# Kernel optimization log

Measured on AMD Instinct MI355X. Metric: run time of the kernel, lower is better.

The kernel has to match this reference:

```python
import jax, jax.numpy as jnp
import numpy as np

D_IN = 1024
D_OUT = 1024
NUM_HEADS = 16
HEAD_DIM = D_OUT // NUM_HEADS


def setup_inputs() -> dict:
    key = jax.random.key(0)
    ks = jax.random.split(key, 6)
    scale = 0.02
    x = jax.random.normal(ks[0], (2, 2048, D_IN), dtype=jnp.float32)
    Wq = jax.random.normal(ks[1], (D_IN, D_OUT), dtype=jnp.float32) * scale
    Wk = jax.random.normal(ks[2], (D_IN, D_OUT), dtype=jnp.float32) * scale
    Wv = jax.random.normal(ks[3], (D_IN, D_OUT), dtype=jnp.float32) * scale
    Wo = jax.random.normal(ks[4], (D_OUT, D_OUT), dtype=jnp.float32) * scale
    bo = jax.random.normal(ks[5], (D_OUT,), dtype=jnp.float32) * scale
    return {"x": x, "Wq": Wq, "Wk": Wk, "Wv": Wv, "Wo": Wo, "bo": bo}


def reference(x, Wq, Wk, Wv, Wo, bo):
    b, T, _ = x.shape
    h, dh = NUM_HEADS, HEAD_DIM
    # QKV projections (no bias), split heads: [b,T,d_out] -> [b,h,T,dh]
    q = (x @ Wq).reshape(b, T, h, dh).transpose(0, 2, 1, 3)
    k = (x @ Wk).reshape(b, T, h, dh).transpose(0, 2, 1, 3)
    v = (x @ Wv).reshape(b, T, h, dh).transpose(0, 2, 1, 3)
    # scaled dot-product scores with causal mask
    scores = jnp.einsum("bhqd,bhkd->bhqk", q, k) / jnp.sqrt(jnp.float32(dh))
    causal = jnp.tril(jnp.ones((T, T), dtype=bool))  # True = allowed
    scores = jnp.where(causal, scores, -jnp.inf)
    attn = jax.nn.softmax(scores, axis=-1)
    # dropout p=0.0 -> identity
    ctx = jnp.einsum("bhqk,bhkd->bhqd", attn, v)
    ctx = ctx.transpose(0, 2, 1, 3).reshape(b, T, h * dh)
    return ctx @ Wo + bo
```

## Files before the change

kernel.cpp:

```cpp
#include <hip/hip_runtime.h>

typedef __attribute__((ext_vector_type(8))) __bf16 bf16x8;
typedef __attribute__((ext_vector_type(4))) __bf16 bf16x4;
typedef __attribute__((ext_vector_type(4))) float  f32x4;

static constexpr int TSEQ    = 2048;
static constexpr int DMODEL  = 1024;
static constexpr int HD      = 64;
static constexpr int VSTRIDE = 2080;
static constexpr int LSTR    = 72;

__global__ __launch_bounds__(256) void k_convert_x(const float* __restrict__ x,
                                                   __bf16* __restrict__ xbf) {
  size_t i = ((size_t)blockIdx.x * 256 + threadIdx.x) * 4;
  float4 v = *(const float4*)(x + i);
  bf16x4 o = { (__bf16)v.x, (__bf16)v.y, (__bf16)v.z, (__bf16)v.w };
  *(bf16x4*)(xbf + i) = o;
}

__global__ __launch_bounds__(1024) void k_transpose_w(const float* __restrict__ w0,
    const float* __restrict__ w1, const float* __restrict__ w2,
    const float* __restrict__ w3, __bf16* __restrict__ wt_all) {
  __shared__ float tile[32][33];
  const float* w = blockIdx.z == 0 ? w0 : blockIdx.z == 1 ? w1 : blockIdx.z == 2 ? w2 : w3;
  __bf16* out = wt_all + (size_t)blockIdx.z * DMODEL * DMODEL;
  int n0 = blockIdx.x * 32, k0 = blockIdx.y * 32;
  int tx = threadIdx.x, ty = threadIdx.y;
  tile[ty][tx] = w[(size_t)(k0 + ty) * DMODEL + n0 + tx];
  __syncthreads();
  out[(size_t)(n0 + ty) * DMODEL + k0 + tx] = (__bf16)tile[tx][ty];
}

__device__ __forceinline__ void gemm_mainloop(const __bf16* __restrict__ A,
                                              const __bf16* __restrict__ Bt,
                                              int bm, int bn,
                                              __bf16* At, __bf16* Bl,
                                              f32x4 acc[4][4]) {
  const int tid  = threadIdx.x;
  const int lane = tid & 63;
  const int l15  = lane & 15, quad = lane >> 4;
  const int wv   = tid >> 6;
  const int wm   = (wv >> 1) * 64, wn = (wv & 1) * 64;
  const int s0   = wv * 2;
  const int srow = lane >> 2;
  const int scol = (lane & 3) << 3;
  for (int k0 = 0; k0 < 1024; k0 += 32) {
    __syncthreads();
#pragma unroll
    for (int ss = 0; ss < 2; ss++) {
      const int s   = s0 + ss;
      const int row = s * 16 + srow;
      const __bf16* ga = A  + (size_t)(bm + row) * 1024 + k0 + scol;
      const __bf16* gb = Bt + (size_t)(bn + row) * 1024 + k0 + scol;
      __builtin_amdgcn_global_load_lds(
          (const __attribute__((address_space(1))) void*)ga,
          (__attribute__((address_space(3))) void*)(At + s * 512), 16, 0, 0);
      __builtin_amdgcn_global_load_lds(
          (const __attribute__((address_space(1))) void*)gb,
          (__attribute__((address_space(3))) void*)(Bl + s * 512), 16, 0, 0);
    }
    __syncthreads();
    bf16x8 af[4], bfr[4];
#pragma unroll
    for (int mt = 0; mt < 4; mt++)
      af[mt] = *(const bf16x8*)(At + (wm + mt * 16 + l15) * 32 + quad * 8);
#pragma unroll
    for (int nt = 0; nt < 4; nt++)
      bfr[nt] = *(const bf16x8*)(Bl + (wn + nt * 16 + l15) * 32 + quad * 8);
#pragma unroll
    for (int mt = 0; mt < 4; mt++)
#pragma unroll
      for (int nt = 0; nt < 4; nt++)
        acc[mt][nt] = __builtin_amdgcn_mfma_f32_16x16x32_bf16(
            af[mt], bfr[nt], acc[mt][nt], 0, 0, 0);
  }
}

__global__ __launch_bounds__(256) void k_gemm_qkv(const __bf16* __restrict__ xbf,
    const __bf16* __restrict__ wt_all, __bf16* __restrict__ qws,
    __bf16* __restrict__ kws, __bf16* __restrict__ vtws) {
  __shared__ __bf16 At[128 * 32];
  __shared__ __bf16 Bl[128 * 32];
  const int which = blockIdx.z;
  const __bf16* wt = wt_all + (size_t)which * DMODEL * DMODEL;
  const int bm = blockIdx.y * 128, bn = blockIdx.x * 128;
  f32x4 acc[4][4];
  const f32x4 z = {0.f, 0.f, 0.f, 0.f};
#pragma unroll
  for (int mt = 0; mt < 4; mt++)
#pragma unroll
    for (int nt = 0; nt < 4; nt++) acc[mt][nt] = z;
  gemm_mainloop(xbf, wt, bm, bn, At, Bl, acc);
  const int lane = threadIdx.x & 63;
  const int l15 = lane & 15, quad = lane >> 4;
  const int wv = threadIdx.x >> 6;
  const int wm = (wv >> 1) * 64, wn = (wv & 1) * 64;
#pragma unroll
  for (int mt = 0; mt < 4; mt++)
#pragma unroll
    for (int nt = 0; nt < 4; nt++)
#pragma unroll
      for (int r = 0; r < 4; r++) {
        int m = bm + wm + mt * 16 + quad * 4 + r;
        int n = bn + wn + nt * 16 + l15;
        int b = m >> 11, t = m & 2047;
        int h = n >> 6,  d = n & 63;
        int bh = b * 16 + h;
        float av = acc[mt][nt][r];
        if (which == 0)      qws[((size_t)bh * TSEQ + t) * HD + d] = (__bf16)(av * 0.125f);
        else if (which == 1) kws[((size_t)bh * TSEQ + t) * HD + d] = (__bf16)av;
        else                 vtws[((size_t)bh * HD + d) * VSTRIDE + t] = (__bf16)av;
      }
}

__global__ __launch_bounds__(256) void k_attn(const __bf16* __restrict__ qws,
    const __bf16* __restrict__ kws, const __bf16* __restrict__ vtws,
    __bf16* __restrict__ ctx) {
  const int qb0 = blockIdx.x, qb1 = 31 - qb0;
  const int bh  = blockIdx.y;
  const int tid = threadIdx.x;
  const int lane = tid & 63, wv = tid >> 6;
  const int l15 = lane & 15, quad = lane >> 4;
  const __bf16* qp = qws  + (size_t)bh * TSEQ * HD;
  const __bf16* kp = kws  + (size_t)bh * TSEQ * HD;
  const __bf16* vp = vtws + (size_t)bh * HD * VSTRIDE;
  const int b = bh >> 4, h = bh & 15;

  __shared__ __bf16 kbuf[2][64 * LSTR];
  __shared__ __bf16 vbuf[2][64 * LSTR];
  __shared__ __bf16 plds[4][16 * 68];

  const f32x4 z = {0.f, 0.f, 0.f, 0.f};
  const int sr = tid >> 3, sc = (tid & 7) * 8;

  const int qr0a = qb0 * 64 + wv * 16;
  const int qr0b = qb1 * 64 + wv * 16;
  bf16x8 aq0[2], aq1[2];
#pragma unroll
  for (int kb = 0; kb < 2; kb++) {
    aq0[kb] = *(const bf16x8*)(qp + (size_t)(qr0a + l15) * HD + kb * 32 + quad * 8);
    aq1[kb] = *(const bf16x8*)(qp + (size_t)(qr0b + l15) * HD + kb * 32 + quad * 8);
  }

  bf16x8 kreg[2], vreg[2];
  kreg[0] = *(const bf16x8*)(kp + (size_t)sr * HD + sc);
  kreg[1] = *(const bf16x8*)(kp + (size_t)(sr + 32) * HD + sc);
  vreg[0] = *(const bf16x8*)(vp + (size_t)sr * VSTRIDE + sc);
  vreg[1] = *(const bf16x8*)(vp + (size_t)(sr + 32) * VSTRIDE + sc);
  *(bf16x8*)(kbuf[0] + sr * LSTR + sc)        = kreg[0];
  *(bf16x8*)(kbuf[0] + (sr + 32) * LSTR + sc) = kreg[1];
  *(bf16x8*)(vbuf[0] + sr * LSTR + sc)        = vreg[0];
  *(bf16x8*)(vbuf[0] + (sr + 32) * LSTR + sc) = vreg[1];
  __syncthreads();

  float lpart[4] = {0.f, 0.f, 0.f, 0.f};
  f32x4 acc[4];
#pragma unroll
  for (int dt = 0; dt < 4; dt++) acc[dt] = z;

  for (int s = 0; s < 33; s++) {
    const int cur = s & 1;
    const bool h0 = (s <= qb0);
    const bool masked = (s == qb0) || (s == 32);

    if (s + 1 < 33) {
      const int ktn = (s + 1 <= qb0) ? (s + 1) * 64 : (s - qb0) * 64;
      kreg[0] = *(const bf16x8*)(kp + (size_t)(ktn + sr) * HD + sc);
      kreg[1] = *(const bf16x8*)(kp + (size_t)(ktn + sr + 32) * HD + sc);
      vreg[0] = *(const bf16x8*)(vp + (size_t)sr * VSTRIDE + ktn + sc);
      vreg[1] = *(const bf16x8*)(vp + (size_t)(sr + 32) * VSTRIDE + ktn + sc);
    }

    const __bf16* kb_ = kbuf[cur];
    const __bf16* vb_ = vbuf[cur];
    f32x4 sarr[4];
#pragma unroll
    for (int nt = 0; nt < 4; nt++) sarr[nt] = z;
#pragma unroll
    for (int nt = 0; nt < 4; nt++)
#pragma unroll
      for (int kb = 0; kb < 2; kb++) {
        bf16x8 bk = *(const bf16x8*)(kb_ + (nt * 16 + l15) * LSTR + kb * 32 + quad * 8);
        bf16x8 a  = h0 ? aq0[kb] : aq1[kb];
        sarr[nt] = __builtin_amdgcn_mfma_f32_16x16x32_bf16(a, bk, sarr[nt], 0, 0, 0);
      }
    if (masked) {
#pragma unroll
      for (int r = 0; r < 4; r++) {
        const int qloc = wv * 16 + quad * 4 + r;
#pragma unroll
        for (int nt = 0; nt < 4; nt++) {
          int kloc = nt * 16 + l15;
          float p = (kloc <= qloc) ? __expf(sarr[nt][r]) : 0.f;
          lpart[r] += p;
          plds[wv][(quad * 4 + r) * 68 + nt * 16 + l15] = (__bf16)p;
        }
      }
    } else {
#pragma unroll
      for (int r = 0; r < 4; r++)
#pragma unroll
        for (int nt = 0; nt < 4; nt++) {
          float p = __expf(sarr[nt][r]);
          lpart[r] += p;
          plds[wv][(quad * 4 + r) * 68 + nt * 16 + l15] = (__bf16)p;
        }
    }
#pragma unroll
    for (int kb = 0; kb < 2; kb++) {
      bf16x8 ap = *(const bf16x8*)(&plds[wv][l15 * 68 + kb * 32 + quad * 8]);
#pragma unroll
      for (int dt = 0; dt < 4; dt++) {
        bf16x8 bvv = *(const bf16x8*)(vb_ + (dt * 16 + l15) * LSTR + kb * 32 + quad * 8);
        acc[dt] = __builtin_amdgcn_mfma_f32_16x16x32_bf16(ap, bvv, acc[dt], 0, 0, 0);
      }
    }

    if (s + 1 < 33) {
      const int nxt = cur ^ 1;
      *(bf16x8*)(kbuf[nxt] + sr * LSTR + sc)        = kreg[0];
      *(bf16x8*)(kbuf[nxt] + (sr + 32) * LSTR + sc) = kreg[1];
      *(bf16x8*)(vbuf[nxt] + sr * LSTR + sc)        = vreg[0];
      *(bf16x8*)(vbuf[nxt] + (sr + 32) * LSTR + sc) = vreg[1];
    }
    __syncthreads();

    if (masked) {
      const int qr0 = h0 ? qr0a : qr0b;
#pragma unroll
      for (int r = 0; r < 4; r++) {
        float l = lpart[r];
        l += __shfl_xor(l, 1, 64);
        l += __shfl_xor(l, 2, 64);
        l += __shfl_xor(l, 4, 64);
        l += __shfl_xor(l, 8, 64);
        float linv = 1.f / l;
        const int qrow = qr0 + quad * 4 + r;
#pragma unroll
        for (int dt = 0; dt < 4; dt++)
          ctx[((size_t)(b * TSEQ + qrow)) * DMODEL + h * 64 + dt * 16 + l15] =
              (__bf16)(acc[dt][r] * linv);
        lpart[r] = 0.f;
      }
#pragma unroll
      for (int dt = 0; dt < 4; dt++) acc[dt] = z;
    }
  }
}

__global__ __launch_bounds__(256) void k_gemm_out(const __bf16* __restrict__ ctx,
    const __bf16* __restrict__ wot, const float* __restrict__ bo,
    float* __restrict__ out) {
  __shared__ __bf16 At[128 * 32];
  __shared__ __bf16 Bl[128 * 32];
  const int bm = blockIdx.y * 128, bn = blockIdx.x * 128;
  f32x4 acc[4][4];
  const f32x4 z = {0.f, 0.f, 0.f, 0.f};
#pragma unroll
  for (int mt = 0; mt < 4; mt++)
#pragma unroll
    for (int nt = 0; nt < 4; nt++) acc[mt][nt] = z;
  gemm_mainloop(ctx, wot, bm, bn, At, Bl, acc);
  const int lane = threadIdx.x & 63;
  const int l15 = lane & 15, quad = lane >> 4;
  const int wv = threadIdx.x >> 6;
  const int wm = (wv >> 1) * 64, wn = (wv & 1) * 64;
#pragma unroll
  for (int mt = 0; mt < 4; mt++)
#pragma unroll
    for (int nt = 0; nt < 4; nt++)
#pragma unroll
      for (int r = 0; r < 4; r++) {
        int m = bm + wm + mt * 16 + quad * 4 + r;
        int n = bn + wn + nt * 16 + l15;
        out[(size_t)m * DMODEL + n] = acc[mt][nt][r] + bo[n];
      }
}

extern "C" void kernel_launch(void* const* d_in, const int* in_sizes, int n_in,
                              void* d_out, int out_size, void* d_ws, size_t ws_size,
                              hipStream_t stream) {
  const float* x  = (const float*)d_in[0];
  const float* Wq = (const float*)d_in[1];
  const float* Wk = (const float*)d_in[2];
  const float* Wv = (const float*)d_in[3];
  const float* Wo = (const float*)d_in[4];
  const float* bo = (const float*)d_in[5];
  float* out = (float*)d_out;

  __bf16* xbf  = (__bf16*)d_ws;
  __bf16* wt   = xbf  + (size_t)4096 * 1024;
  __bf16* qws  = wt   + (size_t)4 * 1024 * 1024;
  __bf16* kws  = qws  + (size_t)32 * 2048 * 64;
  __bf16* vtws = kws  + (size_t)32 * 2048 * 64;
  __bf16* ctx  = xbf;

  k_convert_x<<<4096, 256, 0, stream>>>(x, xbf);
  k_transpose_w<<<dim3(32, 32, 4), dim3(32, 32), 0, stream>>>(Wq, Wk, Wv, Wo, wt);
  k_gemm_qkv<<<dim3(8, 32, 3), 256, 0, stream>>>(xbf, wt, qws, kws, vtws);
  k_attn<<<dim3(16, 32), 256, 0, stream>>>(qws, kws, vtws, ctx);
  k_gemm_out<<<dim3(8, 32), 256, 0, stream>>>(ctx, wt + (size_t)3 * 1024 * 1024, bo, out);
}
```

Baseline: 199.6 us.

## Store V row-major, transpose into swizzled LDS, triple-buffer K/V tiles

The QKV GEMM now writes V in the same [bh,T,64] row-major layout as K, which replaces the strided transposed global stores. The attention kernel instead transposes V while writing it to LDS, using an XOR swizzle to limit bank conflicts, and reads it back with the matching swizzle. K/V staging moves from double to triple buffering, with global loads issued two tiles ahead in alternating register sets. The per-step __syncthreads is replaced by an lgkmcnt wait plus s_barrier. The risks are scalar 2-byte LDS stores for the V transpose, higher register pressure, and the correctness of the hand-written barrier and swizzle.

```diff
diff --git a/kernel.cpp b/kernel.cpp
--- a/kernel.cpp
+++ b/kernel.cpp
@@ -4,11 +4,10 @@
 typedef __attribute__((ext_vector_type(4))) __bf16 bf16x4;
 typedef __attribute__((ext_vector_type(4))) float  f32x4;
 
-static constexpr int TSEQ    = 2048;
-static constexpr int DMODEL  = 1024;
-static constexpr int HD      = 64;
-static constexpr int VSTRIDE = 2080;
-static constexpr int LSTR    = 72;
+static constexpr int TSEQ   = 2048;
+static constexpr int DMODEL = 1024;
+static constexpr int HD     = 64;
+static constexpr int LSTR   = 72;
 
 __global__ __launch_bounds__(256) void k_convert_x(const float* __restrict__ x,
                                                    __bf16* __restrict__ xbf) {
@@ -78,7 +77,7 @@
 
 __global__ __launch_bounds__(256) void k_gemm_qkv(const __bf16* __restrict__ xbf,
     const __bf16* __restrict__ wt_all, __bf16* __restrict__ qws,
-    __bf16* __restrict__ kws, __bf16* __restrict__ vtws) {
+    __bf16* __restrict__ kws, __bf16* __restrict__ vws) {
   __shared__ __bf16 At[128 * 32];
   __shared__ __bf16 Bl[128 * 32];
   const int which = blockIdx.z;
@@ -109,29 +108,30 @@
         float av = acc[mt][nt][r];
         if (which == 0)      qws[((size_t)bh * TSEQ + t) * HD + d] = (__bf16)(av * 0.125f);
         else if (which == 1) kws[((size_t)bh * TSEQ + t) * HD + d] = (__bf16)av;
-        else                 vtws[((size_t)bh * HD + d) * VSTRIDE + t] = (__bf16)av;
+        else                 vws[((size_t)bh * TSEQ + t) * HD + d] = (__bf16)av;
       }
 }
 
 __global__ __launch_bounds__(256) void k_attn(const __bf16* __restrict__ qws,
-    const __bf16* __restrict__ kws, const __bf16* __restrict__ vtws,
+    const __bf16* __restrict__ kws, const __bf16* __restrict__ vws,
     __bf16* __restrict__ ctx) {
   const int qb0 = blockIdx.x, qb1 = 31 - qb0;
   const int bh  = blockIdx.y;
   const int tid = threadIdx.x;
   const int lane = tid & 63, wv = tid >> 6;
   const int l15 = lane & 15, quad = lane >> 4;
-  const __bf16* qp = qws  + (size_t)bh * TSEQ * HD;
-  const __bf16* kp = kws  + (size_t)bh * TSEQ * HD;
-  const __bf16* vp = vtws + (size_t)bh * HD * VSTRIDE;
+  const __bf16* qp = qws + (size_t)bh * TSEQ * HD;
+  const __bf16* kp = kws + (size_t)bh * TSEQ * HD;
+  const __bf16* vp = vws + (size_t)bh * TSEQ * HD;
   const int b = bh >> 4, h = bh & 15;
 
-  __shared__ __bf16 kbuf[2][64 * LSTR];
-  __shared__ __bf16 vbuf[2][64 * LSTR];
-  __shared__ __bf16 plds[4][16 * 68];
+  __shared__ __bf16 kbuf[3][64 * LSTR];
+  __shared__ __bf16 vbuf[3][64 * LSTR];
+  __shared__ __bf16 plds[4][16 * LSTR];
 
   const f32x4 z = {0.f, 0.f, 0.f, 0.f};
-  const int sr = tid >> 3, sc = (tid & 7) * 8;
+  const int sr = tid >> 3;
+  const int sc = (tid & 7) * 8;
 
   const int qr0a = qb0 * 64 + wv * 16;
   const int qr0b = qb1 * 64 + wv * 16;
@@ -142,37 +142,42 @@
     aq1[kb] = *(const bf16x8*)(qp + (size_t)(qr0b + l15) * HD + kb * 32 + quad * 8);
   }
 
-  bf16x8 kreg[2], vreg[2];
-  kreg[0] = *(const bf16x8*)(kp + (size_t)sr * HD + sc);
-  kreg[1] = *(const bf16x8*)(kp + (size_t)(sr + 32) * HD + sc);
-  vreg[0] = *(const bf16x8*)(vp + (size_t)sr * VSTRIDE + sc);
-  vreg[1] = *(const bf16x8*)(vp + (size_t)(sr + 32) * VSTRIDE + sc);
-  *(bf16x8*)(kbuf[0] + sr * LSTR + sc)        = kreg[0];
-  *(bf16x8*)(kbuf[0] + (sr + 32) * LSTR + sc) = kreg[1];
-  *(bf16x8*)(vbuf[0] + sr * LSTR + sc)        = vreg[0];
-  *(bf16x8*)(vbuf[0] + (sr + 32) * LSTR + sc) = vreg[1];
-  __syncthreads();
-
   float lpart[4] = {0.f, 0.f, 0.f, 0.f};
   f32x4 acc[4];
 #pragma unroll
   for (int dt = 0; dt < 4; dt++) acc[dt] = z;
 
-  for (int s = 0; s < 33; s++) {
-    const int cur = s & 1;
+  bf16x8 kA0, kA1, vA0, vA1;
+  bf16x8 kB0, kB1, vB0, vB1;
+
+  auto load_tile = [&](int g, bf16x8& k0, bf16x8& k1, bf16x8& v0, bf16x8& v1) {
+    const int kt = (g <= qb0 ? g : g - qb0 - 1) * 64;
+    k0 = *(const bf16x8*)(kp + (size_t)(kt + sr) * HD + sc);
+    k1 = *(const bf16x8*)(kp + (size_t)(kt + sr + 32) * HD + sc);
+    v0 = *(const bf16x8*)(vp + (size_t)(kt + sr) * HD + sc);
+    v1 = *(const bf16x8*)(vp + (size_t)(kt + sr + 32) * HD + sc);
+  };
+  auto store_tile = [&](int buf, const bf16x8& k0, const bf16x8& k1,
+                        const bf16x8& v0, const bf16x8& v1) {
+    *(bf16x8*)(kbuf[buf] + sr * LSTR + sc)        = k0;
+    *(bf16x8*)(kbuf[buf] + (sr + 32) * LSTR + sc) = k1;
+    const int t0 = sr ^ sc, t1 = (sr + 32) ^ sc;
+#pragma unroll
+    for (int j = 0; j < 8; j++) {
+      vbuf[buf][(sc + j) * LSTR + t0] = v0[j];
+      vbuf[buf][(sc + j) * LSTR + t1] = v1[j];
+    }
+  };
+  auto lgkm_barrier = []() {
+    asm volatile("s_waitcnt lgkmcnt(0)\n\ts_barrier" ::: "memory");
+  };
+
+  auto compute_tile = [&](int s) {
+    const int cu = s % 3;
+    const __bf16* kb_ = kbuf[cu];
+    const __bf16* vb_ = vbuf[cu];
     const bool h0 = (s <= qb0);
     const bool masked = (s == qb0) || (s == 32);
-
-    if (s + 1 < 33) {
-      const int ktn = (s + 1 <= qb0) ? (s + 1) * 64 : (s - qb0) * 64;
-      kreg[0] = *(const bf16x8*)(kp + (size_t)(ktn + sr) * HD + sc);
-      kreg[1] = *(const bf16x8*)(kp + (size_t)(ktn + sr + 32) * HD + sc);
-      vreg[0] = *(const bf16x8*)(vp + (size_t)sr * VSTRIDE + ktn + sc);
-      vreg[1] = *(const bf16x8*)(vp + (size_t)(sr + 32) * VSTRIDE + ktn + sc);
-    }
-
-    const __bf16* kb_ = kbuf[cur];
-    const __bf16* vb_ = vbuf[cur];
     f32x4 sarr[4];
 #pragma unroll
     for (int nt = 0; nt < 4; nt++) sarr[nt] = z;
@@ -181,8 +186,8 @@
 #pragma unroll
       for (int kb = 0; kb < 2; kb++) {
         bf16x8 bk = *(const bf16x8*)(kb_ + (nt * 16 + l15) * LSTR + kb * 32 + quad * 8);
-        bf16x8 a  = h0 ? aq0[kb] : aq1[kb];
-        sarr[nt] = __builtin_amdgcn_mfma_f32_16x16x32_bf16(a, bk, sarr[nt], 0, 0, 0);
+        sarr[nt] = __builtin_amdgcn_mfma_f32_16x16x32_bf16(
+            h0 ? aq0[kb] : aq1[kb], bk, sarr[nt], 0, 0, 0);
       }
     if (masked) {
 #pragma unroll
@@ -193,7 +198,7 @@
           int kloc = nt * 16 + l15;
           float p = (kloc <= qloc) ? __expf(sarr[nt][r]) : 0.f;
           lpart[r] += p;
-          plds[wv][(quad * 4 + r) * 68 + nt * 16 + l15] = (__bf16)p;
+          plds[wv][(quad * 4 + r) * LSTR + nt * 16 + l15] = (__bf16)p;
         }
       }
     } else {
@@ -203,30 +208,25 @@
         for (int nt = 0; nt < 4; nt++) {
           float p = __expf(sarr[nt][r]);
           lpart[r] += p;
-          plds[wv][(quad * 4 + r) * 68 + nt * 16 + l15] = (__bf16)p;
+          plds[wv][(quad * 4 + r) * LSTR + nt * 16 + l15] = (__bf16)p;
         }
     }
 #pragma unroll
     for (int kb = 0; kb < 2; kb++) {
-      bf16x8 ap = *(const bf16x8*)(&plds[wv][l15 * 68 + kb * 32 + quad * 8]);
+      bf16x8 ap = *(const bf16x8*)(&plds[wv][l15 * LSTR + kb * 32 + quad * 8]);
 #pragma unroll
       for (int dt = 0; dt < 4; dt++) {
-        bf16x8 bvv = *(const bf16x8*)(vb_ + (dt * 16 + l15) * LSTR + kb * 32 + quad * 8);
+        const int d = dt * 16 + l15;
+        const int e = ((dt * 2 + (l15 >> 3)) & 7) * 8;
+        bf16x8 bvv = *(const bf16x8*)(vb_ + d * LSTR + ((kb * 32 + quad * 8) ^ e));
         acc[dt] = __builtin_amdgcn_mfma_f32_16x16x32_bf16(ap, bvv, acc[dt], 0, 0, 0);
       }
     }
-
-    if (s + 1 < 33) {
-      const int nxt = cur ^ 1;
-      *(bf16x8*)(kbuf[nxt] + sr * LSTR + sc)        = kreg[0];
-      *(bf16x8*)(kbuf[nxt] + (sr + 32) * LSTR + sc) = kreg[1];
-      *(bf16x8*)(vbuf[nxt] + sr * LSTR + sc)        = vreg[0];
-      *(bf16x8*)(vbuf[nxt] + (sr + 32) * LSTR + sc) = vreg[1];
-    }
-    __syncthreads();
-
-    if (masked) {
-      const int qr0 = h0 ? qr0a : qr0b;
+  };
+
+  auto finalize = [&](int s) {
+    if ((s == qb0) || (s == 32)) {
+      const int qr0 = (s == 32) ? qr0b : qr0a;
 #pragma unroll
       for (int r = 0; r < 4; r++) {
         float l = lpart[r];
@@ -244,6 +244,31 @@
       }
 #pragma unroll
       for (int dt = 0; dt < 4; dt++) acc[dt] = z;
+    }
+  };
+
+  load_tile(0, kA0, kA1, vA0, vA1);
+  store_tile(0, kA0, kA1, vA0, vA1);
+  load_tile(1, kB0, kB1, vB0, vB1);
+  load_tile(2, kA0, kA1, vA0, vA1);
+  lgkm_barrier();
+
+  for (int sb = 0; sb < 34; sb += 2) {
+    {
+      const int s = sb;
+      compute_tile(s);
+      if (s + 1 < 33) store_tile((s + 1) % 3, kB0, kB1, vB0, vB1);
+      if (s + 3 < 33) load_tile(s + 3, kB0, kB1, vB0, vB1);
+      finalize(s);
+      lgkm_barrier();
+    }
+    if (sb + 1 < 33) {
+      const int s = sb + 1;
+      compute_tile(s);
+      if (s + 1 < 33) store_tile((s + 1) % 3, kA0, kA1, vA0, vA1);
+      if (s + 3 < 33) load_tile(s + 3, kA0, kA1, vA0, vA1);
+      finalize(s);
+      lgkm_barrier();
     }
   }
 }
@@ -288,16 +313,16 @@
   const float* bo = (const float*)d_in[5];
   float* out = (float*)d_out;
 
-  __bf16* xbf  = (__bf16*)d_ws;
-  __bf16* wt   = xbf  + (size_t)4096 * 1024;
-  __bf16* qws  = wt   + (size_t)4 * 1024 * 1024;
-  __bf16* kws  = qws  + (size_t)32 * 2048 * 64;
-  __bf16* vtws = kws  + (size_t)32 * 2048 * 64;
-  __bf16* ctx  = xbf;
+  __bf16* xbf = (__bf16*)d_ws;
+  __bf16* wt  = xbf + (size_t)4096 * 1024;
+  __bf16* qws = wt  + (size_t)4 * 1024 * 1024;
+  __bf16* kws = qws + (size_t)32 * 2048 * 64;
+  __bf16* vws = kws + (size_t)32 * 2048 * 64;
+  __bf16* ctx = xbf;
 
   k_convert_x<<<4096, 256, 0, stream>>>(x, xbf);
   k_transpose_w<<<dim3(32, 32, 4), dim3(32, 32), 0, stream>>>(Wq, Wk, Wv, Wo, wt);
-  k_gemm_qkv<<<dim3(8, 32, 3), 256, 0, stream>>>(xbf, wt, qws, kws, vtws);
-  k_attn<<<dim3(16, 32), 256, 0, stream>>>(qws, kws, vtws, ctx);
+  k_gemm_qkv<<<dim3(8, 32, 3), 256, 0, stream>>>(xbf, wt, qws, kws, vws);
+  k_attn<<<dim3(16, 32), 256, 0, stream>>>(qws, kws, vws, ctx);
   k_gemm_out<<<dim3(8, 32), 256, 0, stream>>>(ctx, wt + (size_t)3 * 1024 * 1024, bo, out);
 }
```

New measurement: 220.0 us. 1.1x slower.
